# Kernel tuning notes

Hardware: AMD Instinct MI355X
Metric: run time of the kernel (lower is better)

## Reference

```python
import jax, jax.numpy as jnp
import numpy as np

H, V, B, T = 2048, 32000, 8, 256
G = 4          # num_generations per reward group
BETA = 0.1     # KL coefficient
EPS = 1e-4


def setup_inputs() -> dict:
    key = jax.random.key(0)
    ks = jax.random.split(key, 6)
    scale = 1.0 / np.sqrt(H)  # keep logits O(1) so exp() in KL is finite
    return {
        "x": jax.random.normal(ks[0], (B, T, H), jnp.float32),
        "weight": jax.random.normal(ks[1], (V, H), jnp.float32) * scale,
        "attention_mask": jax.random.randint(ks[2], (B, T), 0, 2).astype(jnp.int32),
        "rewards": jax.random.normal(ks[3], (B,), jnp.float32),
        "ref_input": jax.random.normal(ks[4], (B, T, H), jnp.float32),
        "ref_weight": jax.random.normal(ks[5], (V, H), jnp.float32) * scale,
    }


def _gather_token_logps(inp, w, tokens):
    # log-softmax over vocab, then gather at `tokens`  -> (B, T)
    logits = jnp.einsum('bth,vh->btv', inp, w)
    logp = jax.nn.log_softmax(logits, axis=-1)
    return jnp.take_along_axis(logp, tokens[..., None], axis=-1)[..., 0]


def reference(x, weight, attention_mask, rewards, ref_input, ref_weight):
    # policy logits / log-probs  (B, T, V)
    logits = jnp.einsum('bth,vh->btv', x, weight)
    logp = jax.nn.log_softmax(logits, axis=-1)
    # chosen tokens = argmax of policy logits (as in the Liger test harness)
    tokens = jnp.argmax(logits, axis=-1)                                   # (B, T) int
    tok_logp = jnp.take_along_axis(logp, tokens[..., None], axis=-1)[..., 0]  # (B, T)

    # reference model log-probs at the same tokens (no grad)
    ref_tok_logp = jax.lax.stop_gradient(
        _gather_token_logps(ref_input, ref_weight, tokens))               # (B, T)

    # group-relative advantages (groups of G generations, unbiased std as torch.std)
    r = rewards.reshape(-1, G)
    mean_g = jnp.repeat(r.mean(axis=1), G)                                # (B,)
    std_g = jnp.repeat(r.std(axis=1, ddof=1), G)                          # (B,)
    adv = (rewards - mean_g) / (std_g + EPS)                              # (B,)

    # ratio = exp(logp - logp.detach()) == 1 in value, carries grad of logp
    per_tok = jnp.exp(tok_logp - jax.lax.stop_gradient(tok_logp)) * adv[:, None]
    # k3 KL estimator vs reference policy
    kl = jnp.exp(ref_tok_logp - tok_logp) - (ref_tok_logp - tok_logp) - 1.0
    per_tok = per_tok - BETA * kl

    mask = attention_mask.astype(jnp.float32)
    loss = -(per_tok * mask).sum() / mask.sum()
    mean_kl = ((kl * mask).sum(axis=1) / mask.sum(axis=1)).mean()
    return loss, mean_kl
```

## Files before the change

kernel.cpp:

```cpp
#include <hip/hip_runtime.h>
#include <hip/hip_bf16.h>
#include <math.h>

#define H_DIM 2048
#define V_DIM 32000
#define BT    2048
#define TM    128
#define TN    128
#define TK    32
#define NBLK  (V_DIM / TN)
#define BETA  0.1f
#define EPSR  1e-4f

typedef __attribute__((ext_vector_type(8))) short bf16x8;
typedef __attribute__((ext_vector_type(4))) float f32x4;

__device__ __forceinline__ unsigned pack_bf16x2(float a, float b) {
    unsigned ua = __float_as_uint(a) + 0x8000u;
    unsigned ub = __float_as_uint(b) + 0x8000u;
    return __builtin_amdgcn_perm(ub, ua, 0x07060302u);
}

__device__ __forceinline__ void merge_ms(float& m, float& s, float m2, float s2) {
    float nm = fmaxf(m, m2);
    s = s * __expf(m - nm) + s2 * __expf(m2 - nm);
    m = nm;
}

__global__ __launch_bounds__(256) void gemm_lse_kernel(
    const float* __restrict__ A,
    const float* __restrict__ Bw,
    float4* __restrict__ part,
    const int* __restrict__ token,
    float* __restrict__ gather_out)
{
    __shared__ char smem[TM*TK*2 + TN*TK*2];
    ushort* sA = (ushort*)smem;
    ushort* sB = (ushort*)(smem + TM*TK*2);
    float* redM   = (float*)smem;
    float* redS   = (float*)(smem + 1024);
    int*   redC   = (int*)  (smem + 2048);
    int*   tokloc = (int*)  (smem + 3072);

    const int tid  = threadIdx.x;
    const int lane = tid & 63;
    const int wv   = tid >> 6;
    const int wm   = wv >> 1, wn = wv & 1;
    const int q    = lane >> 4, cl = lane & 15;

    const int m0 = blockIdx.x * TM;
    const int n0 = blockIdx.y * TN;
    const int nb = blockIdx.y;

    const int srow = tid >> 1;
    const int sseg = tid & 1;
    const float4* gA = (const float4*)(A  + (size_t)(m0 + srow) * H_DIM) + sseg * 4;
    const float4* gB = (const float4*)(Bw + (size_t)(n0 + srow) * H_DIM) + sseg * 4;
    uint4* wA = (uint4*)sA + srow * 4 + sseg * 2;
    uint4* wB = (uint4*)sB + srow * 4 + sseg * 2;

    f32x4 acc[4][4];
    const f32x4 zero = {0.f, 0.f, 0.f, 0.f};
    #pragma unroll
    for (int i = 0; i < 4; i++)
        #pragma unroll
        for (int j = 0; j < 4; j++) acc[i][j] = zero;

    float4 ra0 = gA[0], ra1 = gA[1], ra2 = gA[2], ra3 = gA[3];
    float4 rb0 = gB[0], rb1 = gB[1], rb2 = gB[2], rb3 = gB[3];

    for (int kt = 0; kt < H_DIM; kt += TK) {
        wA[0] = make_uint4(pack_bf16x2(ra0.x,ra0.y), pack_bf16x2(ra0.z,ra0.w),
                           pack_bf16x2(ra1.x,ra1.y), pack_bf16x2(ra1.z,ra1.w));
        wA[1] = make_uint4(pack_bf16x2(ra2.x,ra2.y), pack_bf16x2(ra2.z,ra2.w),
                           pack_bf16x2(ra3.x,ra3.y), pack_bf16x2(ra3.z,ra3.w));
        wB[0] = make_uint4(pack_bf16x2(rb0.x,rb0.y), pack_bf16x2(rb0.z,rb0.w),
                           pack_bf16x2(rb1.x,rb1.y), pack_bf16x2(rb1.z,rb1.w));
        wB[1] = make_uint4(pack_bf16x2(rb2.x,rb2.y), pack_bf16x2(rb2.z,rb2.w),
                           pack_bf16x2(rb3.x,rb3.y), pack_bf16x2(rb3.z,rb3.w));
        __syncthreads();

        if (kt + TK < H_DIM) {
            int kq = (kt + TK) >> 2;
            ra0 = gA[kq]; ra1 = gA[kq+1]; ra2 = gA[kq+2]; ra3 = gA[kq+3];
            rb0 = gB[kq]; rb1 = gB[kq+1]; rb2 = gB[kq+2]; rb3 = gB[kq+3];
        }

        bf16x8 af[4], bfr[4];
        #pragma unroll
        for (int i = 0; i < 4; i++) {
            af[i]  = *(const bf16x8*)(sA + (wm*64 + i*16 + cl) * TK + q*8);
            bfr[i] = *(const bf16x8*)(sB + (wn*64 + i*16 + cl) * TK + q*8);
        }
        #pragma unroll
        for (int i = 0; i < 4; i++)
            #pragma unroll
            for (int j = 0; j < 4; j++)
                acc[i][j] = __builtin_amdgcn_mfma_f32_16x16x32_bf16(af[i], bfr[j], acc[i][j], 0, 0, 0);
        __syncthreads();
    }

    #pragma unroll
    for (int ti = 0; ti < 4; ti++) {
        #pragma unroll
        for (int r = 0; r < 4; r++) {
            float vals[4];
            #pragma unroll
            for (int j = 0; j < 4; j++) vals[j] = acc[ti][j][r];
            float m = vals[0]; int cj = 0;
            #pragma unroll
            for (int j = 1; j < 4; j++) if (vals[j] > m) { m = vals[j]; cj = j; }
            float s = 0.f;
            #pragma unroll
            for (int j = 0; j < 4; j++) s += __expf(vals[j] - m);
            int cidx = wn*64 + cj*16 + cl;
            #pragma unroll
            for (int off = 1; off < 16; off <<= 1) {
                float m2 = __shfl_xor(m, off);
                float s2 = __shfl_xor(s, off);
                int   c2 = __shfl_xor(cidx, off);
                float nm = fmaxf(m, m2);
                s = s * __expf(m - nm) + s2 * __expf(m2 - nm);
                if (m2 > m || (m2 == m && c2 < cidx)) cidx = c2;
                m = nm;
            }
            int rloc = wm*64 + ti*16 + q*4 + r;
            if (cl == 0) { redM[rloc*2+wn] = m; redS[rloc*2+wn] = s; redC[rloc*2+wn] = cidx; }
        }
    }
    __syncthreads();
    if (tid < TM) {
        float ma = redM[tid*2+0], mb = redM[tid*2+1];
        float sa = redS[tid*2+0], sb = redS[tid*2+1];
        int   ca = redC[tid*2+0], cb = redC[tid*2+1];
        float nm = fmaxf(ma, mb);
        float s  = sa * __expf(ma - nm) + sb * __expf(mb - nm);
        int   cc = (mb > ma || (mb == ma && cb < ca)) ? cb : ca;
        part[(size_t)(m0 + tid) * NBLK + nb] = make_float4(nm, s, __int_as_float(n0 + cc), 0.f);
    }

    if (token != nullptr) {
        if (tid < TM) tokloc[tid] = token[m0 + tid] - n0;
        __syncthreads();
        #pragma unroll
        for (int ti = 0; ti < 4; ti++) {
            #pragma unroll
            for (int r = 0; r < 4; r++) {
                int rloc = wm*64 + ti*16 + q*4 + r;
                int tl = tokloc[rloc];
                if (tl >= 0 && tl < TN && ((tl >> 6) & 1) == wn && (tl & 15) == cl) {
                    int tjm = (tl >> 4) & 3;
                    float v = acc[ti][0][r];
                    if (tjm == 1) v = acc[ti][1][r];
                    if (tjm == 2) v = acc[ti][2][r];
                    if (tjm == 3) v = acc[ti][3][r];
                    gather_out[m0 + rloc] = v;
                }
            }
        }
    }
}

__global__ __launch_bounds__(256) void reduce_policy_kernel(
    const float4* __restrict__ part, int* __restrict__ token, float* __restrict__ tok_logp)
{
    int row = blockIdx.x, t = threadIdx.x;
    float m = -3.0e38f, s = 0.f; int cc = 0x7fffffff;
    if (t < NBLK) { float4 p = part[(size_t)row * NBLK + t]; m = p.x; s = p.y; cc = __float_as_int(p.z); }
    for (int off = 1; off < 64; off <<= 1) {
        float m2 = __shfl_xor(m, off);
        float s2 = __shfl_xor(s, off);
        int   c2 = __shfl_xor(cc, off);
        float nm = fmaxf(m, m2);
        s = s * __expf(m - nm) + s2 * __expf(m2 - nm);
        if (m2 > m || (m2 == m && c2 < cc)) cc = c2;
        m = nm;
    }
    __shared__ float smM[4], smS[4]; __shared__ int smC[4];
    if ((t & 63) == 0) { smM[t>>6] = m; smS[t>>6] = s; smC[t>>6] = cc; }
    __syncthreads();
    if (t == 0) {
        m = smM[0]; s = smS[0]; cc = smC[0];
        for (int i = 1; i < 4; i++) {
            float m2 = smM[i], s2 = smS[i]; int c2 = smC[i];
            float nm = fmaxf(m, m2);
            s = s * __expf(m - nm) + s2 * __expf(m2 - nm);
            if (m2 > m || (m2 == m && c2 < cc)) cc = c2;
            m = nm;
        }
        token[row] = cc;
        tok_logp[row] = -__logf(s);
    }
}

__global__ __launch_bounds__(256) void reduce_ref_kernel(
    const float4* __restrict__ part, const float* __restrict__ tok_logp,
    const float* __restrict__ gathered, float* __restrict__ klrow)
{
    int row = blockIdx.x, t = threadIdx.x;
    float m = -3.0e38f, s = 0.f;
    if (t < NBLK) { float4 p = part[(size_t)row * NBLK + t]; m = p.x; s = p.y; }
    for (int off = 1; off < 64; off <<= 1) {
        float m2 = __shfl_xor(m, off), s2 = __shfl_xor(s, off);
        merge_ms(m, s, m2, s2);
    }
    __shared__ float smM[4], smS[4];
    if ((t & 63) == 0) { smM[t>>6] = m; smS[t>>6] = s; }
    __syncthreads();
    if (t == 0) {
        m = smM[0]; s = smS[0];
        for (int i = 1; i < 4; i++) merge_ms(m, s, smM[i], smS[i]);
        float lse = m + __logf(s);
        float d = (gathered[row] - lse) - tok_logp[row];
        klrow[row] = __expf(d) - d - 1.0f;
    }
}

__global__ __launch_bounds__(256) void final_kernel(
    const int* __restrict__ amask, const float* __restrict__ rewards,
    const float* __restrict__ klrow, float* __restrict__ out)
{
    int t = threadIdx.x;
    int b = t >> 5;
    int g = b >> 2;
    float r0 = rewards[g*4+0], r1 = rewards[g*4+1], r2 = rewards[g*4+2], r3 = rewards[g*4+3];
    float mean = 0.25f * (r0 + r1 + r2 + r3);
    float var = ((r0-mean)*(r0-mean) + (r1-mean)*(r1-mean) +
                 (r2-mean)*(r2-mean) + (r3-mean)*(r3-mean)) * (1.0f/3.0f);
    float adv = (rewards[b] - mean) / (sqrtf(var) + EPSR);

    float ln = 0.f, ms = 0.f, kb = 0.f, mb = 0.f;
    for (int i = 0; i < 8; i++) {
        int row = t*8 + i;
        float mk = (float)amask[row];
        float kl = klrow[row];
        ln += (adv - BETA * kl) * mk;
        ms += mk;
        kb += kl * mk;
        mb += mk;
    }
    __shared__ float sLN[256], sMS[256], sKB[256], sMB[256], sKLb[8];
    sLN[t] = ln; sMS[t] = ms; sKB[t] = kb; sMB[t] = mb;
    __syncthreads();
    if (t < 8) {
        float skb = 0.f, smb = 0.f;
        for (int i = 0; i < 32; i++) { skb += sKB[t*32+i]; smb += sMB[t*32+i]; }
        sKLb[t] = skb / smb;
    }
    __syncthreads();
    if (t == 0) {
        float lnt = 0.f, mst = 0.f;
        for (int i = 0; i < 256; i++) { lnt += sLN[i]; mst += sMS[i]; }
        float mkl = 0.f;
        for (int i = 0; i < 8; i++) mkl += sKLb[i];
        out[0] = -lnt / mst;
        out[1] = mkl * 0.125f;
    }
}

extern "C" void kernel_launch(void* const* d_in, const int* in_sizes, int n_in,
                              void* d_out, int out_size, void* d_ws, size_t ws_size,
                              hipStream_t stream)
{
    const float* x       = (const float*)d_in[0];
    const float* w       = (const float*)d_in[1];
    const int*   amask   = (const int*)  d_in[2];
    const float* rewards = (const float*)d_in[3];
    const float* rx      = (const float*)d_in[4];
    const float* rw      = (const float*)d_in[5];
    float* out = (float*)d_out;

    char* ws = (char*)d_ws;
    const size_t PART_BYTES = (size_t)BT * NBLK * sizeof(float4);
    float4* part     = (float4*)ws;
    int*    token    = (int*)  (ws + PART_BYTES);
    float*  tok_logp = (float*)(ws + PART_BYTES + 8192);
    float*  gathered = (float*)(ws + PART_BYTES + 16384);
    float*  klrow    = (float*)(ws + PART_BYTES + 24576);

    dim3 g(BT / TM, NBLK), blk(256);
    gemm_lse_kernel<<<g, blk, 0, stream>>>(x, w, part, nullptr, nullptr);
    reduce_policy_kernel<<<BT, 256, 0, stream>>>(part, token, tok_logp);
    gemm_lse_kernel<<<g, blk, 0, stream>>>(rx, rw, part, token, gathered);
    reduce_ref_kernel<<<BT, 256, 0, stream>>>(part, tok_logp, gathered, klrow);
    final_kernel<<<1, 256, 0, stream>>>(amask, rewards, klrow, out);
}
```

Before: 1.680 ms.

## Pre-pack inputs to bf16 tiles and use direct global-to-LDS loads in fused GEMM

```diff
diff --git a/kernel.cpp b/kernel.cpp
--- a/kernel.cpp
+++ b/kernel.cpp
@@ -8,12 +8,14 @@
 #define TM    128
 #define TN    128
 #define TK    32
+#define NKT   (H_DIM / TK)
 #define NBLK  (V_DIM / TN)
 #define BETA  0.1f
 #define EPSR  1e-4f
 
 typedef __attribute__((ext_vector_type(8))) short bf16x8;
 typedef __attribute__((ext_vector_type(4))) float f32x4;
+
 
 __device__ __forceinline__ unsigned pack_bf16x2(float a, float b) {
     unsigned ua = __float_as_uint(a) + 0x8000u;
@@ -27,11 +29,136 @@
     m = nm;
 }
 
-__global__ __launch_bounds__(256) void gemm_lse_kernel(
-    const float* __restrict__ A,
-    const float* __restrict__ Bw,
-    float4* __restrict__ part,
-    const int* __restrict__ token,
+__device__ __forceinline__ void gl_lds16(const void* g, void* l) {
+    __builtin_amdgcn_global_load_lds(
+        (const __attribute__((address_space(1))) void*)g,
+        (__attribute__((address_space(3))) void*)l, 16, 0, 0);
+}
+
+__global__ __launch_bounds__(256) void pack_kernel(
+    const float* __restrict__ src, uint4* __restrict__ dst)
+{
+    __shared__ float tile[128 * 40];
+    const int t  = threadIdx.x;
+    const int rt = blockIdx.x, kt = blockIdx.y;
+
+    #pragma unroll
+    for (int it = 0; it < 4; it++) {
+        int idx = (it * 256 + t) * 4;
+        int row = idx >> 5, k = idx & 31;
+        float4 v = *(const float4*)(src + (size_t)(rt * 128 + row) * H_DIM + kt * 32 + k);
+        *(float4*)(tile + row * 40 + k) = v;
+    }
+    __syncthreads();
+
+    uint4* d = dst + ((size_t)(rt * 64 + kt) << 9);
+    #pragma unroll
+    for (int it = 0; it < 2; it++) {
+        int c = it * 256 + t;
+        int kq = c >> 7, row = c & 127;
+        const float* p = tile + row * 40 + kq * 8;
+        d[c] = make_uint4(pack_bf16x2(p[0], p[1]), pack_bf16x2(p[2], p[3]),
+                          pack_bf16x2(p[4], p[5]), pack_bf16x2(p[6], p[7]));
+    }
+}
+
+__global__ __launch_bounds__(256) void gemm_lse_fast(
+    const ushort* __restrict__ Ap, const ushort* __restrict__ Wp,
+    const ushort* __restrict__ Rp, const ushort* __restrict__ RWp,
+    float4* __restrict__ part, float4* __restrict__ part2)
+{
+    __shared__ char smem[16384];
+    float* redM = (float*)smem;
+    float* redS = (float*)(smem + 1024);
+    int*   redC = (int*)  (smem + 2048);
+
+    const int tid  = threadIdx.x;
+    const int lane = tid & 63;
+    const int wv   = tid >> 6;
+    const int wm   = wv >> 1, wn = wv & 1;
+    const int q    = lane >> 4, cl = lane & 15;
+
+    const int mb = blockIdx.x, nb = blockIdx.y;
+    const ushort* A  = blockIdx.z ? Rp  : Ap;
+    const ushort* Bw = blockIdx.z ? RWp : Wp;
+    float4* pp = blockIdx.z ? part2 : part;
+
+    const ushort* gs = (wv < 2 ? A + (size_t)mb * 64 * 4096
+                               : Bw + (size_t)nb * 64 * 4096)
+                       + (size_t)(wv & 1) * 4 * 512 + lane * 8;
+    char* ls = smem + (wv < 2 ? 0 : 8192) + (wv & 1) * 4 * 1024 + lane * 16;
+
+    f32x4 acc[4][4];
+    const f32x4 zero = {0.f, 0.f, 0.f, 0.f};
+    #pragma unroll
+    for (int i = 0; i < 4; i++)
+        #pragma unroll
+        for (int j = 0; j < 4; j++) acc[i][j] = zero;
+
+    for (int kt = 0; kt < NKT; kt++) {
+        #pragma unroll
+        for (int c = 0; c < 4; c++) gl_lds16(gs + c * 512, ls + c * 1024);
+        gs += 4096;
+        __syncthreads();
+
+        bf16x8 af[4], bfr[4];
+        #pragma unroll
+        for (int i = 0; i < 4; i++) {
+            af[i]  = *(const bf16x8*)(smem + (q * 128 + wm * 64 + i * 16 + cl) * 16);
+            bfr[i] = *(const bf16x8*)(smem + 8192 + (q * 128 + wn * 64 + i * 16 + cl) * 16);
+        }
+        #pragma unroll
+        for (int i = 0; i < 4; i++)
+            #pragma unroll
+            for (int j = 0; j < 4; j++)
+                acc[i][j] = __builtin_amdgcn_mfma_f32_16x16x32_bf16(af[i], bfr[j], acc[i][j], 0, 0, 0);
+        __syncthreads();
+    }
+
+    #pragma unroll
+    for (int ti = 0; ti < 4; ti++) {
+        #pragma unroll
+        for (int r = 0; r < 4; r++) {
+            float vals[4];
+            #pragma unroll
+            for (int j = 0; j < 4; j++) vals[j] = acc[ti][j][r];
+            float m = vals[0]; int cj = 0;
+            #pragma unroll
+            for (int j = 1; j < 4; j++) if (vals[j] > m) { m = vals[j]; cj = j; }
+            float s = 0.f;
+            #pragma unroll
+            for (int j = 0; j < 4; j++) s += __expf(vals[j] - m);
+            int cidx = wn * 64 + cj * 16 + cl;
+            #pragma unroll
+            for (int off = 1; off < 16; off <<= 1) {
+                float m2 = __shfl_xor(m, off);
+                float s2 = __shfl_xor(s, off);
+                int   c2 = __shfl_xor(cidx, off);
+                float nm = fmaxf(m, m2);
+                s = s * __expf(m - nm) + s2 * __expf(m2 - nm);
+                if (m2 > m || (m2 == m && c2 < cidx)) cidx = c2;
+                m = nm;
+            }
+            int rloc = wm * 64 + ti * 16 + q * 4 + r;
+            if (cl == 0) { redM[rloc*2+wn] = m; redS[rloc*2+wn] = s; redC[rloc*2+wn] = cidx; }
+        }
+    }
+    __syncthreads();
+    if (tid < TM) {
+        float ma = redM[tid*2+0], mb2 = redM[tid*2+1];
+        float sa = redS[tid*2+0], sb  = redS[tid*2+1];
+        int   ca = redC[tid*2+0], cb  = redC[tid*2+1];
+        float nm = fmaxf(ma, mb2);
+        float s  = sa * __expf(ma - nm) + sb * __expf(mb2 - nm);
+        int   cc = (mb2 > ma || (mb2 == ma && cb < ca)) ? cb : ca;
+        pp[(size_t)(mb * TM + tid) * NBLK + nb] =
+            make_float4(nm, s, __int_as_float(nb * TN + cc), 0.f);
+    }
+}
+
+__global__ __launch_bounds__(256) void gemm_lse_fallback(
+    const float* __restrict__ A, const float* __restrict__ Bw,
+    float4* __restrict__ part, const int* __restrict__ token,
     float* __restrict__ gather_out)
 {
     __shared__ char smem[TM*TK*2 + TN*TK*2];
@@ -47,13 +174,11 @@
     const int wv   = tid >> 6;
     const int wm   = wv >> 1, wn = wv & 1;
     const int q    = lane >> 4, cl = lane & 15;
-
     const int m0 = blockIdx.x * TM;
     const int n0 = blockIdx.y * TN;
     const int nb = blockIdx.y;
 
-    const int srow = tid >> 1;
-    const int sseg = tid & 1;
+    const int srow = tid >> 1, sseg = tid & 1;
     const float4* gA = (const float4*)(A  + (size_t)(m0 + srow) * H_DIM) + sseg * 4;
     const float4* gB = (const float4*)(Bw + (size_t)(n0 + srow) * H_DIM) + sseg * 4;
     uint4* wA = (uint4*)sA + srow * 4 + sseg * 2;
@@ -79,13 +204,11 @@
         wB[1] = make_uint4(pack_bf16x2(rb2.x,rb2.y), pack_bf16x2(rb2.z,rb2.w),
                            pack_bf16x2(rb3.x,rb3.y), pack_bf16x2(rb3.z,rb3.w));
         __syncthreads();
-
         if (kt + TK < H_DIM) {
             int kq = (kt + TK) >> 2;
             ra0 = gA[kq]; ra1 = gA[kq+1]; ra2 = gA[kq+2]; ra3 = gA[kq+3];
             rb0 = gB[kq]; rb1 = gB[kq+1]; rb2 = gB[kq+2]; rb3 = gB[kq+3];
         }
-
         bf16x8 af[4], bfr[4];
         #pragma unroll
         for (int i = 0; i < 4; i++) {
@@ -161,6 +284,7 @@
     }
 }
 
+
 __global__ __launch_bounds__(256) void reduce_policy_kernel(
     const float4* __restrict__ part, int* __restrict__ token, float* __restrict__ tok_logp)
 {
@@ -193,6 +317,23 @@
     }
 }
 
+__global__ __launch_bounds__(256) void dot_gather_kernel(
+    const float* __restrict__ rx, const float* __restrict__ rw,
+    const int* __restrict__ token, float* __restrict__ out)
+{
+    int row = blockIdx.x, t = threadIdx.x;
+    const float4* a = (const float4*)(rx + (size_t)row * H_DIM);
+    const float4* b = (const float4*)(rw + (size_t)token[row] * H_DIM);
+    float4 a0 = a[t*2], a1 = a[t*2+1], b0 = b[t*2], b1 = b[t*2+1];
+    float s = a0.x*b0.x + a0.y*b0.y + a0.z*b0.z + a0.w*b0.w
+            + a1.x*b1.x + a1.y*b1.y + a1.z*b1.z + a1.w*b1.w;
+    for (int off = 1; off < 64; off <<= 1) s += __shfl_xor(s, off);
+    __shared__ float ss[4];
+    if ((t & 63) == 0) ss[t >> 6] = s;
+    __syncthreads();
+    if (t == 0) out[row] = ss[0] + ss[1] + ss[2] + ss[3];
+}
+
 __global__ __launch_bounds__(256) void reduce_ref_kernel(
     const float4* __restrict__ part, const float* __restrict__ tok_logp,
     const float* __restrict__ gathered, float* __restrict__ klrow)
@@ -258,6 +399,7 @@
     }
 }
 
+
 extern "C" void kernel_launch(void* const* d_in, const int* in_sizes, int n_in,
                               void* d_out, int out_size, void* d_ws, size_t ws_size,
                               hipStream_t stream)
@@ -269,19 +411,49 @@
     const float* rx      = (const float*)d_in[4];
     const float* rw      = (const float*)d_in[5];
     float* out = (float*)d_out;
-
     char* ws = (char*)d_ws;
-    const size_t PART_BYTES = (size_t)BT * NBLK * sizeof(float4);
-    float4* part     = (float4*)ws;
-    int*    token    = (int*)  (ws + PART_BYTES);
-    float*  tok_logp = (float*)(ws + PART_BYTES + 8192);
-    float*  gathered = (float*)(ws + PART_BYTES + 16384);
-    float*  klrow    = (float*)(ws + PART_BYTES + 24576);
-
-    dim3 g(BT / TM, NBLK), blk(256);
-    gemm_lse_kernel<<<g, blk, 0, stream>>>(x, w, part, nullptr, nullptr);
-    reduce_policy_kernel<<<BT, 256, 0, stream>>>(part, token, tok_logp);
-    gemm_lse_kernel<<<g, blk, 0, stream>>>(rx, rw, part, token, gathered);
-    reduce_ref_kernel<<<BT, 256, 0, stream>>>(part, tok_logp, gathered, klrow);
-    final_kernel<<<1, 256, 0, stream>>>(amask, rewards, klrow, out);
-}
+
+    const size_t W_P  = (size_t)V_DIM * H_DIM * 2;
+    const size_t A_P  = (size_t)BT * H_DIM * 2;
+    const size_t PART = (size_t)BT * NBLK * 16;
+    const size_t NEED = 2*W_P + 2*A_P + 2*PART + 4*8192;
+
+    if (ws_size >= NEED) {
+        ushort* Wp   = (ushort*)(ws);
+        ushort* RWp  = (ushort*)(ws + W_P);
+        ushort* Ap   = (ushort*)(ws + 2*W_P);
+        ushort* Rp   = (ushort*)(ws + 2*W_P + A_P);
+        float4* part  = (float4*)(ws + 2*W_P + 2*A_P);
+        float4* part2 = (float4*)(ws + 2*W_P + 2*A_P + PART);
+        char*   tail  =          ws + 2*W_P + 2*A_P + 2*PART;
+        int*   token    = (int*)  (tail);
+        float* tok_logp = (float*)(tail + 8192);
+        float* gathered = (float*)(tail + 16384);
+        float* klrow    = (float*)(tail + 24576);
+
+        pack_kernel<<<dim3(BT/128,  NKT), 256, 0, stream>>>(x,  (uint4*)Ap);
+        pack_kernel<<<dim3(V_DIM/128, NKT), 256, 0, stream>>>(w,  (uint4*)Wp);
+        pack_kernel<<<dim3(BT/128,  NKT), 256, 0, stream>>>(rx, (uint4*)Rp);
+        pack_kernel<<<dim3(V_DIM/128, NKT), 256, 0, stream>>>(rw, (uint4*)RWp);
+
+        gemm_lse_fast<<<dim3(BT/TM, NBLK, 2), 256, 0, stream>>>(Ap, Wp, Rp, RWp, part, part2);
+
+        reduce_policy_kernel<<<BT, 256, 0, stream>>>(part, token, tok_logp);
+        dot_gather_kernel<<<BT, 256, 0, stream>>>(rx, rw, token, gathered);
+        reduce_ref_kernel<<<BT, 256, 0, stream>>>(part2, tok_logp, gathered, klrow);
+        final_kernel<<<1, 256, 0, stream>>>(amask, rewards, klrow, out);
+    } else {
+        float4* part     = (float4*)ws;
+        int*    token    = (int*)  (ws + PART);
+        float*  tok_logp = (float*)(ws + PART + 8192);
+        float*  gathered = (float*)(ws + PART + 16384);
+        float*  klrow    = (float*)(ws + PART + 24576);
+
+        dim3 g(BT / TM, NBLK), blk(256);
+        gemm_lse_fallback<<<g, blk, 0, stream>>>(x, w, part, nullptr, nullptr);
+        reduce_policy_kernel<<<BT, 256, 0, stream>>>(part, token, tok_logp);
+        gemm_lse_fallback<<<g, blk, 0, stream>>>(rx, rw, part, token, gathered);
+        reduce_ref_kernel<<<BT, 256, 0, stream>>>(part, tok_logp, gathered, klrow);
+        final_kernel<<<1, 256, 0, stream>>>(amask, rewards, klrow, out);
+    }
+}
```

After: 1.363 ms. 1.23x faster.
